# Kernel tuning notes

Hardware: AMD Instinct MI355X
Metric: run time of the kernel (lower is better)

The kernel has to match this reference:

```python
import jax, jax.numpy as jnp
import numpy as np

B, T, IN = 1048576, 4, 2
SPIN, TRAIN = 1000, 500000  # spinLen, traintimeLen


def setup_inputs() -> dict:
    key = jax.random.key(0)
    ks = jax.random.split(key, 5)
    return {
        "x": jax.random.normal(ks[0], (B, T, IN), jnp.float32),
        "y_obs": jax.random.normal(ks[1], (B, 1), jnp.float32),
        "weight_r_yom": jax.random.uniform(ks[2], (1, 1), jnp.float32),
        "weight_r_ylm": jax.random.uniform(ks[3], (1, 1), jnp.float32),
        "weight_r_yfm": jax.random.uniform(ks[4], (1, 1), jnp.float32),
        "epoch": 1,
        "time_lag": 0,
    }


def _forward(x, y_obs, wom, wlm, wfm, time_lag):
    # x: (B, T, 2) batch_first; module transposes and loops b (outer), t (inner)
    Bn, Tn, _ = x.shape
    # constant softmax-derived gates (hidden_size = 1 -> scalars)
    denom = jnp.exp(wom) + jnp.exp(wlm) + jnp.exp(wfm)
    oo = (jnp.exp(wom) / denom).reshape(())
    ol = (jnpp := jnp.exp(wlm) / denom).reshape(()) if False else (jnp.exp(wlm) / denom).reshape(())
    f = 1.0 - oo - ol
    # flattened linear recurrence: c_after[k] = f * c_after[k-1] + u[k], c_after[-1]=0
    u = x[time_lag:, :, 0].reshape(-1)  # ((B - time_lag) * T,)
    a = f * jnp.ones_like(u)

    def combine(e1, e2):
        a1, b1 = e1
        a2, b2 = e2
        return a1 * a2, a2 * b1 + b2

    _, c_after = jax.lax.associative_scan(combine, (a, u))
    c_before = jnp.concatenate([jnp.zeros((1,), u.dtype), c_after[:-1]])
    # the module records c_0 / h_0 / l_0 at the LAST t iteration of each b,
    # i.e., the carry just before step index (b - time_lag) * T + (T - 1)
    idx = jnp.arange(Bn - time_lag) * Tn + (Tn - 1)
    c0 = c_before[idx]  # (B - time_lag,)
    c0_full = jnp.concatenate([jnp.zeros((time_lag,), u.dtype), c0])[:, None]  # (B, 1)
    valid = (jnp.arange(Bn) >= time_lag)[:, None]  # rows < time_lag stay zero

    zeros = jnp.zeros((Bn, 1), u.dtype)
    c_n = c0_full                      # zero-padded already for b < time_lag
    q_n = oo * c0_full                 # h_0 (unused in outputs, kept for clarity)
    h_n = oo * c0_full                 # h_0 + bp_0, with bp_0 = 0 (ib = 0)
    l_n = ol * c0_full
    bp_n = zeros
    Gate_ib = zeros
    Gate_oo = jnp.where(valid, oo, 0.0).astype(u.dtype)
    Gate_ol = jnp.where(valid, ol, 0.0).astype(u.dtype)
    Gate_f = jnp.where(valid, f, 0.0).astype(u.dtype)
    obsstd = jnp.std(y_obs[SPIN:TRAIN], ddof=1)  # torch.std is unbiased
    obs_std = jnp.where(valid, obsstd, 0.0).astype(u.dtype)
    h_nout = jnp.concatenate([h_n, obs_std], axis=1)  # (B, 2)
    return (h_n, c_n, l_n, bp_n, Gate_ib, Gate_oo, Gate_ol, Gate_f, h_nout, obs_std)


def reference(x, y_obs, weight_r_yom, weight_r_ylm, weight_r_yfm, epoch, time_lag):
    del epoch  # unused by the module
    return _forward(x, y_obs, weight_r_yom, weight_r_ylm, weight_r_yfm, int(time_lag))
```

## Files before the change

kernel.cpp:

```cpp
#include <hip/hip_runtime.h>


#define SPIN 1000
#define TRAIN 500000
#define NPART 256
#define WIN 64

__global__ void reduce_partial_k(const float* __restrict__ y, int B,
                                 double* __restrict__ part) {
  int hi = TRAIN < B ? TRAIN : B;
  float s = 0.f, s2 = 0.f;
  for (int i = SPIN + blockIdx.x * blockDim.x + threadIdx.x; i < hi;
       i += gridDim.x * blockDim.x) {
    float v = y[i];
    s += v;
    s2 += v * v;
  }
  for (int off = 32; off; off >>= 1) {
    s += __shfl_down(s, off, 64);
    s2 += __shfl_down(s2, off, 64);
  }
  __shared__ float ls[4], ls2[4];
  int t = threadIdx.x;
  if ((t & 63) == 0) { ls[t >> 6] = s; ls2[t >> 6] = s2; }
  __syncthreads();
  if (t == 0) {
    double S = 0, S2 = 0;
    for (int j = 0; j < 4; ++j) { S += ls[j]; S2 += ls2[j]; }
    part[2 * blockIdx.x] = S;
    part[2 * blockIdx.x + 1] = S2;
  }
}

__global__ void finalize_scalars_k(const double* __restrict__ part,
                                   const float* __restrict__ wom,
                                   const float* __restrict__ wlm,
                                   const float* __restrict__ wfm, int B,
                                   float* __restrict__ sc) {
  __shared__ double ss[NPART], ss2[NPART];
  int t = threadIdx.x;
  ss[t] = part[2 * t];
  ss2[t] = part[2 * t + 1];
  __syncthreads();
  for (int off = NPART / 2; off; off >>= 1) {
    if (t < off) { ss[t] += ss[t + off]; ss2[t] += ss2[t + off]; }
    __syncthreads();
  }
  if (t == 0) {
    int hi = TRAIN < B ? TRAIN : B;
    double n = (double)(hi - SPIN);
    double S = ss[0], S2 = ss2[0];
    double var = (S2 - S * S / n) / (n - 1.0);
    float sd = (float)sqrt(var > 0.0 ? var : 0.0);
    float eo = expf(wom[0]), el = expf(wlm[0]), ef = expf(wfm[0]);
    float denom = eo + el + ef;
    float oo = eo / denom, ol = el / denom;
    float f = 1.f - oo - ol;
    sc[0] = oo; sc[1] = ol; sc[2] = f; sc[3] = sd;
  }
}

__global__ void __launch_bounds__(256)
main_out_k(const float* __restrict__ x, const int* __restrict__ tl_p,
           const float* __restrict__ sc, float* __restrict__ out, int B) {
  __shared__ float u[1088];
  const int tl = tl_p[0];
  const float oo = sc[0], ol = sc[1], f = sc[2], sd = sc[3];

  const long b0 = (long)blockIdx.x * 256;
  const long i0 = b0 - tl;
  long k_last = i0 * 4 + 2 + 255 * 4;
  long k_lo = i0 * 4 + 2 - (WIN - 1);
  if (k_lo < 0) k_lo = 0;
  const long kmax = ((long)B - tl) * 4;
  long count = k_last - k_lo + 1;
  if (k_last < 0) count = 0;
  if (count > 1088) count = 1088;

  const int t = threadIdx.x;
  for (long idx = t; idx < count; idx += 256) {
    long k = k_lo + idx;
    float v = 0.f;
    if (k < kmax) v = x[(long)tl * 8 + 2 * k];
    u[idx] = v;
  }
  __syncthreads();

  const long b = b0 + t;
  if (b >= B) return;
  float c0 = 0.f;
  const bool valid = (b >= tl);
  if (valid) {
    long i = b - tl;
    long ke = i * 4 + 2;
    long ks = ke - (WIN - 1);
    if (ks < 0) ks = 0;
    for (long k = ks; k <= ke; ++k) c0 = fmaf(f, c0, u[k - k_lo]);
  }
  const float h = oo * c0;
  const float l = ol * c0;
  const long Bl = B;
  out[b] = h;
  out[Bl + b] = c0;
  out[2 * Bl + b] = l;
  out[3 * Bl + b] = 0.f;
  out[4 * Bl + b] = 0.f;
  out[5 * Bl + b] = valid ? oo : 0.f;
  out[6 * Bl + b] = valid ? ol : 0.f;
  out[7 * Bl + b] = valid ? f : 0.f;
  const float sdm = valid ? sd : 0.f;
  reinterpret_cast<float2*>(out + 8 * Bl)[b] = make_float2(h, sdm);
  out[10 * Bl + b] = sdm;
}

extern "C" void kernel_launch(void* const* d_in, const int* in_sizes, int n_in,
                              void* d_out, int out_size, void* d_ws,
                              size_t ws_size, hipStream_t stream) {
  const float* x = (const float*)d_in[0];
  const float* y_obs = (const float*)d_in[1];
  const float* wom = (const float*)d_in[2];
  const float* wlm = (const float*)d_in[3];
  const float* wfm = (const float*)d_in[4];
  const int* tl = (const int*)d_in[6];
  float* out = (float*)d_out;
  const int B = in_sizes[1];

  float* sc = (float*)d_ws;
  double* part = (double*)((char*)d_ws + 64);

  reduce_partial_k<<<NPART, 256, 0, stream>>>(y_obs, B, part);
  finalize_scalars_k<<<1, NPART, 0, stream>>>(part, wom, wlm, wfm, B, sc);
  const int grid = (B + 255) / 256;
  main_out_k<<<grid, 256, 0, stream>>>(x, tl, sc, out, B);
}
```

Before: 120.7 us.

## Fuse scalar finalize into main kernel and block the recurrence window by four

Removes the single-block finalize kernel. Each main-kernel block now reduces the 256 partial sums itself with a wave shuffle and keeps the gate scalars in shared memory, which saves one launch and one serialized dependency. The truncated recurrence window is regrouped into float4 chunks and evaluated Horner-style with f^4 steps, and the std reduction uses float4 loads. Every block redundantly reads the 256 partials, and the window start is aligned differently, so rounding changes slightly.

After: 112.8 us. 1.07x faster.

```diff
diff --git a/kernel.cpp b/kernel.cpp
--- a/kernel.cpp
+++ b/kernel.cpp
@@ -4,24 +4,28 @@
 #define SPIN 1000
 #define TRAIN 500000
 #define NPART 256
-#define WIN 64
 
-__global__ void reduce_partial_k(const float* __restrict__ y, int B,
-                                 double* __restrict__ part) {
-  int hi = TRAIN < B ? TRAIN : B;
+__global__ void __launch_bounds__(256)
+reduce_partial_k(const float* __restrict__ y, int B, double* __restrict__ part) {
+  const int hi = TRAIN < B ? TRAIN : B;
+  const int q0 = SPIN / 4;
+  const int q1 = hi / 4;
   float s = 0.f, s2 = 0.f;
-  for (int i = SPIN + blockIdx.x * blockDim.x + threadIdx.x; i < hi;
-       i += gridDim.x * blockDim.x) {
-    float v = y[i];
-    s += v;
-    s2 += v * v;
+  const float4* y4 = reinterpret_cast<const float4*>(y);
+  for (int q = q0 + blockIdx.x * 256 + threadIdx.x; q < q1; q += NPART * 256) {
+    float4 v = y4[q];
+    s += v.x + v.y + v.z + v.w;
+    s2 += v.x * v.x + v.y * v.y + v.z * v.z + v.w * v.w;
+  }
+  if (blockIdx.x == 0 && threadIdx.x == 0) {
+    for (int i = q1 * 4; i < hi; ++i) { float v = y[i]; s += v; s2 += v * v; }
   }
   for (int off = 32; off; off >>= 1) {
     s += __shfl_down(s, off, 64);
     s2 += __shfl_down(s2, off, 64);
   }
   __shared__ float ls[4], ls2[4];
-  int t = threadIdx.x;
+  const int t = threadIdx.x;
   if ((t & 63) == 0) { ls[t >> 6] = s; ls2[t >> 6] = s2; }
   __syncthreads();
   if (t == 0) {
@@ -32,76 +36,74 @@
   }
 }
 
-__global__ void finalize_scalars_k(const double* __restrict__ part,
-                                   const float* __restrict__ wom,
-                                   const float* __restrict__ wlm,
-                                   const float* __restrict__ wfm, int B,
-                                   float* __restrict__ sc) {
-  __shared__ double ss[NPART], ss2[NPART];
-  int t = threadIdx.x;
-  ss[t] = part[2 * t];
-  ss2[t] = part[2 * t + 1];
-  __syncthreads();
-  for (int off = NPART / 2; off; off >>= 1) {
-    if (t < off) { ss[t] += ss[t + off]; ss2[t] += ss2[t + off]; }
-    __syncthreads();
-  }
-  if (t == 0) {
-    int hi = TRAIN < B ? TRAIN : B;
-    double n = (double)(hi - SPIN);
-    double S = ss[0], S2 = ss2[0];
-    double var = (S2 - S * S / n) / (n - 1.0);
-    float sd = (float)sqrt(var > 0.0 ? var : 0.0);
-    float eo = expf(wom[0]), el = expf(wlm[0]), ef = expf(wfm[0]);
-    float denom = eo + el + ef;
-    float oo = eo / denom, ol = el / denom;
-    float f = 1.f - oo - ol;
-    sc[0] = oo; sc[1] = ol; sc[2] = f; sc[3] = sd;
-  }
-}
-
 __global__ void __launch_bounds__(256)
-main_out_k(const float* __restrict__ x, const int* __restrict__ tl_p,
-           const float* __restrict__ sc, float* __restrict__ out, int B) {
+main_out_k(const float* __restrict__ x, const double* __restrict__ part,
+           const float* __restrict__ wom, const float* __restrict__ wlm,
+           const float* __restrict__ wfm, const int* __restrict__ tl_p,
+           float* __restrict__ out, int B) {
   __shared__ float u[1088];
-  const int tl = tl_p[0];
-  const float oo = sc[0], ol = sc[1], f = sc[2], sd = sc[3];
-
-  const long b0 = (long)blockIdx.x * 256;
-  const long i0 = b0 - tl;
-  long k_last = i0 * 4 + 2 + 255 * 4;
-  long k_lo = i0 * 4 + 2 - (WIN - 1);
-  if (k_lo < 0) k_lo = 0;
-  const long kmax = ((long)B - tl) * 4;
-  long count = k_last - k_lo + 1;
-  if (k_last < 0) count = 0;
-  if (count > 1088) count = 1088;
+  __shared__ float scal[4];
 
   const int t = threadIdx.x;
-  for (long idx = t; idx < count; idx += 256) {
-    long k = k_lo + idx;
-    float v = 0.f;
-    if (k < kmax) v = x[(long)tl * 8 + 2 * k];
-    u[idx] = v;
+  const int tl = tl_p[0];
+  const int b0 = blockIdx.x * 256;
+  const int i0 = b0 - tl;
+  const int klo4 = 4 * (i0 - 16);
+  const int X0 = tl * 8;
+
+  for (int p = t; p < 544; p += 256) {
+    int k = klo4 + 2 * p;
+    float2 w = make_float2(0.f, 0.f);
+    if (k >= 0) {
+      float4 v = *reinterpret_cast<const float4*>(x + X0 + 2 * k);
+      w = make_float2(v.x, v.z);
+    }
+    *reinterpret_cast<float2*>(&u[2 * p]) = w;
+  }
+
+  if (t < 64) {
+    double S = 0, S2 = 0;
+    for (int j = t; j < NPART; j += 64) { S += part[2 * j]; S2 += part[2 * j + 1]; }
+    for (int m = 32; m; m >>= 1) {
+      S += __shfl_xor(S, m, 64);
+      S2 += __shfl_xor(S2, m, 64);
+    }
+    if (t == 0) {
+      const int hi = TRAIN < B ? TRAIN : B;
+      double n = (double)(hi - SPIN);
+      double var = (S2 - S * S / n) / (n - 1.0);
+      float sd = (float)sqrt(var > 0.0 ? var : 0.0);
+      float eo = expf(wom[0]), el = expf(wlm[0]), ef = expf(wfm[0]);
+      float denom = eo + el + ef;
+      float oo = eo / denom, ol = el / denom;
+      scal[0] = oo; scal[1] = ol; scal[2] = 1.f - oo - ol; scal[3] = sd;
+    }
   }
   __syncthreads();
 
-  const long b = b0 + t;
+  const int b = b0 + t;
   if (b >= B) return;
-  float c0 = 0.f;
+  const float oo = scal[0], ol = scal[1], f = scal[2], sd = scal[3];
+  const float f2 = f * f, f3 = f2 * f, f4 = f2 * f2;
+
+  const float4* uq = reinterpret_cast<const float4*>(u);
+  float c = uq[t].w;
+#pragma unroll
+  for (int m = 1; m <= 15; ++m) {
+    float4 q = uq[t + m];
+    float w = fmaf(fmaf(fmaf(q.x, f, q.y), f, q.z), f, q.w);
+    c = fmaf(f4, c, w);
+  }
+  float4 qf = uq[t + 16];
+  c = fmaf(f3, c, fmaf(fmaf(qf.x, f, qf.y), f, qf.z));
+
   const bool valid = (b >= tl);
-  if (valid) {
-    long i = b - tl;
-    long ke = i * 4 + 2;
-    long ks = ke - (WIN - 1);
-    if (ks < 0) ks = 0;
-    for (long k = ks; k <= ke; ++k) c0 = fmaf(f, c0, u[k - k_lo]);
-  }
-  const float h = oo * c0;
-  const float l = ol * c0;
-  const long Bl = B;
+  if (!valid) c = 0.f;
+  const float h = oo * c;
+  const float l = ol * c;
+  const int Bl = B;
   out[b] = h;
-  out[Bl + b] = c0;
+  out[Bl + b] = c;
   out[2 * Bl + b] = l;
   out[3 * Bl + b] = 0.f;
   out[4 * Bl + b] = 0.f;
@@ -125,11 +127,9 @@
   float* out = (float*)d_out;
   const int B = in_sizes[1];
 
-  float* sc = (float*)d_ws;
-  double* part = (double*)((char*)d_ws + 64);
+  double* part = (double*)d_ws;
 
   reduce_partial_k<<<NPART, 256, 0, stream>>>(y_obs, B, part);
-  finalize_scalars_k<<<1, NPART, 0, stream>>>(part, wom, wlm, wfm, B, sc);
   const int grid = (B + 255) / 256;
-  main_out_k<<<grid, 256, 0, stream>>>(x, tl, sc, out, B);
+  main_out_k<<<grid, 256, 0, stream>>>(x, part, wom, wlm, wfm, tl, out, B);
 }
```
